# Kernel tuning notes

Hardware: AMD Instinct MI355X
Metric: run time of the kernel (lower is better)

The kernel has to match this reference:

```python
import jax, jax.numpy as jnp
import numpy as np

DIM = 768
HEADS = 12
HEAD_DIM = DIM // HEADS
SCALE = HEAD_DIM ** -0.5


def setup_inputs() -> dict:
    key = jax.random.key(0)
    ks = jax.random.split(key, 8)
    B, N, C = 8, 1024, DIM
    s = 0.02
    return {
        "x": jax.random.normal(ks[0], (B, N, C), jnp.float32),
        "y": jax.random.normal(ks[1], (B, N, C), jnp.float32),
        "x_qkv_w": jax.random.normal(ks[2], (3 * C, C), jnp.float32) * s,
        "y_qkv_w": jax.random.normal(ks[3], (3 * C, C), jnp.float32) * s,
        "x_proj_w": jax.random.normal(ks[4], (C, C), jnp.float32) * s,
        "x_proj_b": jnp.zeros((C,), jnp.float32),
        "y_proj_w": jax.random.normal(ks[5], (C, C), jnp.float32) * s,
        "y_proj_b": jnp.zeros((C,), jnp.float32),
    }


def _split_qkv(t, qkv_w):
    # t: [B,N,C] -> q,k,v each [B,H,N,D]
    B, N, C = t.shape
    qkv = t @ qkv_w.T                      # [B,N,3C]
    qkv = qkv.reshape(B, N, 3, HEADS, HEAD_DIM).transpose(2, 0, 3, 1, 4)
    return qkv[0], qkv[1], qkv[2]


def reference(x, y, x_qkv_w, y_qkv_w, x_proj_w, x_proj_b, y_proj_w, y_proj_b):
    B, N, C = x.shape
    x_q, x_k, x_v = _split_qkv(x, x_qkv_w)
    y_q, y_k, y_v = _split_qkv(y, y_qkv_w)

    # scores: [B,H,N,N]; dropout is identity (attn_drop=0)
    x_attn = jax.nn.softmax(jnp.einsum('bhnd,bhmd->bhnm', x_q * SCALE, x_k), axis=-1)
    y_attn = jax.nn.softmax(jnp.einsum('bhnd,bhmd->bhnm', y_q * SCALE, y_k), axis=-1)

    # swapped V aggregation: x-branch attends over y_v, y-branch over x_v
    x_out = jnp.einsum('bhnm,bhmd->bhnd', x_attn, y_v).transpose(0, 2, 1, 3).reshape(B, N, C)
    y_out = jnp.einsum('bhnm,bhmd->bhnd', y_attn, x_v).transpose(0, 2, 1, 3).reshape(B, N, C)

    x_out = x_out @ x_proj_w.T + x_proj_b
    y_out = y_out @ y_proj_w.T + y_proj_b
    return (x_out, y_out)
```

## Files before the change

### kernel.cpp

```cpp
#include <hip/hip_runtime.h>
#include <hip/hip_bf16.h>
#include <stdint.h>
#include <stddef.h>

typedef unsigned short u16;
typedef __attribute__((ext_vector_type(8))) short bf16x8;
typedef __attribute__((ext_vector_type(4))) short bf16x4;
typedef __attribute__((ext_vector_type(4))) float f32x4;
typedef __attribute__((ext_vector_type(4))) unsigned short u16x4;

#define MFMA_BF16 __builtin_amdgcn_mfma_f32_16x16x32_bf16

#if defined(__has_builtin)
#if __has_builtin(__builtin_amdgcn_mfma_f32_16x16x16bf16_1k)
#define MFMA16(a, b, c) __builtin_amdgcn_mfma_f32_16x16x16bf16_1k(a, b, c, 0, 0, 0)
#endif
#endif
#ifndef MFMA16
__device__ __forceinline__ f32x4 mfma16_asm(bf16x4 a, bf16x4 b, f32x4 c) {
  asm volatile("s_nop 1\n\tv_mfma_f32_16x16x16_bf16 %0, %1, %2, %0\n\ts_nop 7\n\ts_nop 7"
               : "+v"(c) : "v"(a), "v"(b));
  return c;
}
#define MFMA16(a, b, c) mfma16_asm(a, b, c)
#endif

#if defined(__has_builtin)
#if __has_builtin(__builtin_amdgcn_exp2f)
#define EXP2F(x) __builtin_amdgcn_exp2f(x)
#endif
#endif
#ifndef EXP2F
#define EXP2F(x) __expf((x) * 0.6931471805599453f)
#endif

#define BAR_FULL asm volatile("s_waitcnt vmcnt(0)\n\ts_barrier" ::: "memory")

#define QSCALE 0.18033688011112042f

__device__ __forceinline__ u16 f2b(float x) {
  uint32_t u = __builtin_bit_cast(uint32_t, x);
  return (u16)((u + 0x7fffu + ((u >> 16) & 1u)) >> 16);
}

__device__ __forceinline__ bf16x4 pack4(float a, float b, float c, float d) {
  union { __hip_bfloat162 h[2]; bf16x4 v; } u;
  u.h[0] = __float22bfloat162_rn(make_float2(a, b));
  u.h[1] = __float22bfloat162_rn(make_float2(c, d));
  return u.v;
}

__device__ __forceinline__ void async16(const void* g, void* l) {
  __builtin_amdgcn_global_load_lds((const __attribute__((address_space(1))) void*)g,
                                   (__attribute__((address_space(3))) void*)l, 16, 0, 0);
}

__global__ void cvt_all(const float* __restrict__ x, const float* __restrict__ y,
                        const float* __restrict__ xqw, const float* __restrict__ yqw,
                        const float* __restrict__ xpw, const float* __restrict__ ypw,
                        u16* __restrict__ dst) {
  long i = ((long)blockIdx.x * 256 + threadIdx.x) * 4;
  const float* src;
  long off;
  if (i < 6291456)       { src = x;   off = 0; }
  else if (i < 12582912) { src = y;   off = 6291456; }
  else if (i < 14352384) { src = xqw; off = 12582912; }
  else if (i < 16121856) { src = yqw; off = 14352384; }
  else if (i < 16711680) { src = xpw; off = 16121856; }
  else                   { src = ypw; off = 16711680; }
  float4 v = *(const float4*)(src + (i - off));
  u16x4 o = { f2b(v.x), f2b(v.y), f2b(v.z), f2b(v.w) };
  *(u16x4*)(dst + i) = o;
}

__global__ __launch_bounds__(256, 2)
void qkv_gemm(const u16* __restrict__ Xb, const u16* __restrict__ Yb,
              const u16* __restrict__ Wx, const u16* __restrict__ Wy,
              u16* __restrict__ Qx, u16* __restrict__ Kx, u16* __restrict__ Vtx,
              u16* __restrict__ Qy, u16* __restrict__ Ky, u16* __restrict__ Vty) {
  __shared__ alignas(16) char smem[65536];
  const int br = blockIdx.z;
  const u16* A = br ? Yb : Xb;
  const u16* W = br ? Wy : Wx;
  u16* Qd = br ? Qy : Qx;
  u16* Kd = br ? Ky : Kx;
  u16* Vd = br ? Vty : Vtx;
  const int m0 = blockIdx.x * 128;
  const int j0 = blockIdx.y * 128;
  const int tid = threadIdx.x;
  const int wave = tid >> 6, lane = tid & 63;
  const int quad = lane >> 4, l16 = lane & 15;
  const int wm = wave >> 1, wn = wave & 1;
  const int srow = wave * 32 + (lane >> 3);
  const int scol = (((lane & 7) ^ ((lane >> 3) & 7)) * 8);
  const int l7 = l16 & 7;

  auto stage = [&](int k0, int p) {
#pragma unroll
    for (int c = 0; c < 4; ++c) {
      async16(A + (size_t)(m0 + srow + c * 8) * 768 + k0 + scol,
              smem + p * 16384 + wave * 4096 + c * 1024);
      async16(W + (size_t)(j0 + srow + c * 8) * 768 + k0 + scol,
              smem + 32768 + p * 16384 + wave * 4096 + c * 1024);
    }
  };

  f32x4 acc[4][4] = {};
  stage(0, 0);

  for (int kt = 0; kt < 12; ++kt) {
    const int p = kt & 1;
    BAR_FULL;
    if (kt < 11) stage((kt + 1) * 64, p ^ 1);
    const u16* Ap = (const u16*)smem + p * 8192;
    const u16* Bp = (const u16*)smem + 16384 + p * 8192;
#pragma unroll
    for (int kc = 0; kc < 2; ++kc) {
      bf16x8 af[4], bfr[4];
#pragma unroll
      for (int t = 0; t < 4; ++t) {
        af[t]  = *(const bf16x8*)&Ap[(wm * 64 + t * 16 + l16) * 64 + (((kc * 4 + quad) ^ l7) * 8)];
        bfr[t] = *(const bf16x8*)&Bp[(wn * 64 + t * 16 + l16) * 64 + (((kc * 4 + quad) ^ l7) * 8)];
      }
#pragma unroll
      for (int mt = 0; mt < 4; ++mt)
#pragma unroll
        for (int nt = 0; nt < 4; ++nt)
          acc[mt][nt] = MFMA_BF16(af[mt], bfr[nt], acc[mt][nt], 0, 0, 0);
    }
  }

  __syncthreads();
  u16* Ts = (u16*)smem;
  const int s3 = j0 / 768;

  if (s3 == 2) {
#pragma unroll
    for (int mt = 0; mt < 4; ++mt)
#pragma unroll
      for (int nt = 0; nt < 4; ++nt) {
        const int j = wn * 64 + nt * 16 + l16;
        const int mb = wm * 64 + mt * 16 + quad * 4;
        u16x4 pk = { f2b(acc[mt][nt][0]), f2b(acc[mt][nt][1]),
                     f2b(acc[mt][nt][2]), f2b(acc[mt][nt][3]) };
        *(u16x4*)&Ts[j * 136 + mb] = pk;
      }
    __syncthreads();
#pragma unroll
    for (int rt = 0; rt < 8; ++rt) {
      const int j = wave * 32 + rt * 4 + (lane >> 4);
      const int mo = (lane & 15) * 8;
      bf16x8 v = *(const bf16x8*)&Ts[j * 136 + mo];
      const int jr = j0 + j - 1536;
      const int h = jr >> 6, d = jr & 63;
      const int gm = m0 + mo;
      const int b = gm >> 10, n = gm & 1023;
      *(bf16x8*)&Vd[((size_t)(b * 12 + h) * 64 + d) * 1024 + n] = v;
    }
  } else {
    const float qs = s3 ? 1.0f : QSCALE;
#pragma unroll
    for (int mt = 0; mt < 4; ++mt)
#pragma unroll
      for (int nt = 0; nt < 4; ++nt) {
        const int j = wn * 64 + nt * 16 + l16;
#pragma unroll
        for (int r = 0; r < 4; ++r) {
          const int m = wm * 64 + mt * 16 + quad * 4 + r;
          Ts[m * 136 + j] = f2b(acc[mt][nt][r] * qs);
        }
      }
    __syncthreads();
    u16* Dd = s3 ? Kd : Qd;
#pragma unroll
    for (int rt = 0; rt < 8; ++rt) {
      const int m = wave * 32 + rt * 4 + (lane >> 4);
      const int jh = (lane >> 3) & 1, jo = (lane & 7) * 8;
      bf16x8 v = *(const bf16x8*)&Ts[m * 136 + jh * 64 + jo];
      const int jr = j0 + jh * 64 + jo - s3 * 768;
      const int h = jr >> 6, d = jr & 63;
      const int gm = m0 + m;
      const int b = gm >> 10, n = gm & 1023;
      *(bf16x8*)&Dd[((size_t)(b * 12 + h) * 1024 + n) * 64 + d] = v;
    }
  }
}

__global__ __launch_bounds__(256, 2)
void attn_kernel(const u16* __restrict__ Qx, const u16* __restrict__ Kx, const u16* __restrict__ Vtx,
                 const u16* __restrict__ Qy, const u16* __restrict__ Ky, const u16* __restrict__ Vty,
                 u16* __restrict__ Ox, u16* __restrict__ Oy) {
  __shared__ alignas(16) u16 Ks[2][64 * 64];
  __shared__ alignas(16) u16 Vs[2][64 * 64];
  const int br = blockIdx.z;
  const u16* Q = br ? Qy : Qx;
  const u16* K = br ? Ky : Kx;
  const u16* V = br ? Vtx : Vty;
  u16* O = br ? Oy : Ox;
  const int bh = blockIdx.y;
  const int q0 = blockIdx.x * 256;
  const int tid = threadIdx.x;
  const int wave = tid >> 6, lane = tid & 63;
  const int quad = lane >> 4, l16 = lane & 15;
  const int l7 = l16 & 7;
  const int r8 = (lane >> 3) & 7;
  const int sw = ((lane & 7) ^ r8) * 8;

  const u16* Qb = Q + (size_t)bh * 65536;
  const u16* Kb = K + (size_t)bh * 65536;
  const u16* Vb = V + (size_t)bh * 65536;

  bf16x8 qf[4][2];
#pragma unroll
  for (int mt = 0; mt < 4; ++mt)
#pragma unroll
    for (int kc = 0; kc < 2; ++kc)
      qf[mt][kc] = *(const bf16x8*)(Qb + (size_t)(q0 + wave * 64 + mt * 16 + l16) * 64 + kc * 32 + quad * 8);

  f32x4 oacc[4][4] = {};
  f32x4 lsum[4] = {};
  bf16x4 ones4;
#pragma unroll
  for (int j = 0; j < 4; ++j) ones4[j] = (short)0x3f80;

  const int krow = wave * 16 + r8;

#pragma unroll
  for (int c = 0; c < 2; ++c) {
    async16(Kb + (size_t)(krow + c * 8) * 64 + sw, (char*)Ks[0] + wave * 2048 + c * 1024);
    async16(Vb + (size_t)(krow + c * 8) * 1024 + sw, (char*)Vs[0] + wave * 2048 + c * 1024);
  }

  for (int it = 0; it < 16; ++it) {
    const int p = it & 1;
    BAR_FULL;
    if (it < 15) {
      const int kv1 = (it + 1) * 64;
#pragma unroll
      for (int c = 0; c < 2; ++c) {
        async16(Kb + (size_t)(kv1 + krow + c * 8) * 64 + sw, (char*)Ks[p ^ 1] + wave * 2048 + c * 1024);
        async16(Vb + (size_t)(krow + c * 8) * 1024 + kv1 + sw, (char*)Vs[p ^ 1] + wave * 2048 + c * 1024);
      }
    }

    const u16* Kp = Ks[p];
    const u16* Vp = Vs[p];

#pragma unroll
    for (int kt = 0; kt < 4; ++kt) {
      f32x4 st[4] = {};
#pragma unroll
      for (int kc = 0; kc < 2; ++kc) {
        bf16x8 kf = *(const bf16x8*)&Kp[(kt * 16 + l16) * 64 + (((kc * 4 + quad) ^ l7) * 8)];
#pragma unroll
        for (int mt = 0; mt < 4; ++mt)
          st[mt] = MFMA_BF16(kf, qf[mt][kc], st[mt], 0, 0, 0);
      }
      bf16x4 pf[4];
#pragma unroll
      for (int mt = 0; mt < 4; ++mt)
        pf[mt] = pack4(EXP2F(st[mt][0]), EXP2F(st[mt][1]),
                       EXP2F(st[mt][2]), EXP2F(st[mt][3]));
      bf16x4 vf[4];
      const int c16 = kt * 2 + (quad >> 1);
      const int hh = (quad & 1) * 4;
#pragma unroll
      for (int dt = 0; dt < 4; ++dt)
        vf[dt] = *(const bf16x4*)&Vp[(dt * 16 + l16) * 64 + ((c16 ^ l7) * 8) + hh];
#pragma unroll
      for (int mt = 0; mt < 4; ++mt) {
#pragma unroll
        for (int dt = 0; dt < 4; ++dt)
          oacc[mt][dt] = MFMA16(pf[mt], vf[dt], oacc[mt][dt]);
        lsum[mt] = MFMA16(pf[mt], ones4, lsum[mt]);
      }
    }
  }

  const int b = bh / 12, h = bh % 12;
#pragma unroll
  for (int mt = 0; mt < 4; ++mt) {
#pragma unroll
    for (int r = 0; r < 4; ++r) {
      const float inv = 1.0f / lsum[mt][r];
      const int qrow = q0 + wave * 64 + mt * 16 + quad * 4 + r;
      const size_t ob = ((size_t)(b * 1024 + qrow)) * 768 + h * 64;
#pragma unroll
      for (int nt = 0; nt < 4; ++nt)
        O[ob + nt * 16 + l16] = f2b(oacc[mt][nt][r] * inv);
    }
  }
}

__global__ __launch_bounds__(256, 2)
void proj_gemm(const u16* __restrict__ Ox, const u16* __restrict__ Oy,
               const u16* __restrict__ Pxw, const u16* __restrict__ Pyw,
               const float* __restrict__ bx, const float* __restrict__ by,
               float* __restrict__ out) {
  __shared__ alignas(16) char smem[65536];
  const int br = blockIdx.z;
  const u16* A = br ? Oy : Ox;
  const u16* W = br ? Pyw : Pxw;
  const float* bias = br ? by : bx;
  float* op = out + (size_t)br * 6291456;
  const int m0 = blockIdx.x * 128;
  const int j0 = blockIdx.y * 128;
  const int tid = threadIdx.x;
  const int wave = tid >> 6, lane = tid & 63;
  const int quad = lane >> 4, l16 = lane & 15;
  const int wm = wave >> 1, wn = wave & 1;
  const int srow = wave * 32 + (lane >> 3);
  const int scol = (((lane & 7) ^ ((lane >> 3) & 7)) * 8);
  const int l7 = l16 & 7;

  auto stage = [&](int k0, int p) {
#pragma unroll
    for (int c = 0; c < 4; ++c) {
      async16(A + (size_t)(m0 + srow + c * 8) * 768 + k0 + scol,
              smem + p * 16384 + wave * 4096 + c * 1024);
      async16(W + (size_t)(j0 + srow + c * 8) * 768 + k0 + scol,
              smem + 32768 + p * 16384 + wave * 4096 + c * 1024);
    }
  };

  f32x4 acc[4][4] = {};
  stage(0, 0);

  for (int kt = 0; kt < 12; ++kt) {
    const int p = kt & 1;
    BAR_FULL;
    if (kt < 11) stage((kt + 1) * 64, p ^ 1);
    const u16* Ap = (const u16*)smem + p * 8192;
    const u16* Bp = (const u16*)smem + 16384 + p * 8192;
#pragma unroll
    for (int kc = 0; kc < 2; ++kc) {
      bf16x8 af[4], bfr[4];
#pragma unroll
      for (int t = 0; t < 4; ++t) {
        af[t]  = *(const bf16x8*)&Ap[(wm * 64 + t * 16 + l16) * 64 + (((kc * 4 + quad) ^ l7) * 8)];
        bfr[t] = *(const bf16x8*)&Bp[(wn * 64 + t * 16 + l16) * 64 + (((kc * 4 + quad) ^ l7) * 8)];
      }
#pragma unroll
      for (int mt = 0; mt < 4; ++mt)
#pragma unroll
        for (int nt = 0; nt < 4; ++nt)
          acc[mt][nt] = MFMA_BF16(af[mt], bfr[nt], acc[mt][nt], 0, 0, 0);
    }
  }

#pragma unroll
  for (int mt = 0; mt < 4; ++mt) {
#pragma unroll
    for (int nt = 0; nt < 4; ++nt) {
      const int j = j0 + wn * 64 + nt * 16 + l16;
      const float bj = bias[j];
#pragma unroll
      for (int r = 0; r < 4; ++r) {
        const int m = m0 + wm * 64 + mt * 16 + quad * 4 + r;
        op[(size_t)m * 768 + j] = acc[mt][nt][r] + bj;
      }
    }
  }
}

extern "C" void kernel_launch(void* const* d_in, const int* in_sizes, int n_in,
                              void* d_out, int out_size, void* d_ws, size_t ws_size,
                              hipStream_t stream) {
  (void)in_sizes; (void)n_in; (void)out_size; (void)ws_size;
  const float* x   = (const float*)d_in[0];
  const float* y   = (const float*)d_in[1];
  const float* xqw = (const float*)d_in[2];
  const float* yqw = (const float*)d_in[3];
  const float* xpw = (const float*)d_in[4];
  const float* xpb = (const float*)d_in[5];
  const float* ypw = (const float*)d_in[6];
  const float* ypb = (const float*)d_in[7];
  float* out = (float*)d_out;

  char* p = (char*)d_ws;
  u16* Xb  = (u16*)p; p += 12582912;
  u16* Yb  = (u16*)p; p += 12582912;
  u16* Wxb = (u16*)p; p += 3538944;
  u16* Wyb = (u16*)p; p += 3538944;
  u16* Pxb = (u16*)p; p += 1179648;
  u16* Pyb = (u16*)p; p += 1179648;
  u16* Qx  = (u16*)p; p += 12582912;
  u16* Kx  = (u16*)p; p += 12582912;
  u16* Vtx = (u16*)p; p += 12582912;
  u16* Qy  = (u16*)p; p += 12582912;
  u16* Ky  = (u16*)p; p += 12582912;
  u16* Vty = (u16*)p; p += 12582912;
  u16* Ox  = Xb;
  u16* Oy  = Yb;

  cvt_all<<<16896, 256, 0, stream>>>(x, y, xqw, yqw, xpw, ypw, Xb);

  qkv_gemm<<<dim3(64, 18, 2), 256, 0, stream>>>(Xb, Yb, Wxb, Wyb,
                                                Qx, Kx, Vtx, Qy, Ky, Vty);
  attn_kernel<<<dim3(4, 96, 2), 256, 0, stream>>>(Qx, Kx, Vtx, Qy, Ky, Vty, Ox, Oy);
  proj_gemm<<<dim3(64, 6, 2), 256, 0, stream>>>(Ox, Oy, Pxb, Pyb, xpb, ypb, out);
}
```

Baseline: 275.6 us.

## Switch attention kernel to 32x32x16 MFMA with permlane32 swap fragment reshuffle

Rewrites the attention inner loop to use 32x32x16 bf16 MFMA for both QK^T and PV instead of 16x16x32 plus 16x16x16. The exp'd scores are repacked into A-operand layout with v_permlane32_swap rather than being fed directly. The row sum is computed with VALU adds instead of an extra MFMA against a ones vector, then reduced across half-waves and shared through LDS. Launch bounds are raised to 3 blocks per CU to increase occupancy. The larger MFMA tiles are meant to cut instruction count and LDS fragment loads, at the cost of shuffle overhead and more register pressure under the tighter occupancy bound.

```diff
diff --git a/kernel.cpp b/kernel.cpp
--- a/kernel.cpp
+++ b/kernel.cpp
@@ -7,23 +7,11 @@
 typedef __attribute__((ext_vector_type(8))) short bf16x8;
 typedef __attribute__((ext_vector_type(4))) short bf16x4;
 typedef __attribute__((ext_vector_type(4))) float f32x4;
+typedef __attribute__((ext_vector_type(16))) float f32x16;
 typedef __attribute__((ext_vector_type(4))) unsigned short u16x4;
 
 #define MFMA_BF16 __builtin_amdgcn_mfma_f32_16x16x32_bf16
-
-#if defined(__has_builtin)
-#if __has_builtin(__builtin_amdgcn_mfma_f32_16x16x16bf16_1k)
-#define MFMA16(a, b, c) __builtin_amdgcn_mfma_f32_16x16x16bf16_1k(a, b, c, 0, 0, 0)
-#endif
-#endif
-#ifndef MFMA16
-__device__ __forceinline__ f32x4 mfma16_asm(bf16x4 a, bf16x4 b, f32x4 c) {
-  asm volatile("s_nop 1\n\tv_mfma_f32_16x16x16_bf16 %0, %1, %2, %0\n\ts_nop 7\n\ts_nop 7"
-               : "+v"(c) : "v"(a), "v"(b));
-  return c;
-}
-#define MFMA16(a, b, c) mfma16_asm(a, b, c)
-#endif
+#define MFMA32    __builtin_amdgcn_mfma_f32_32x32x16_bf16
 
 #if defined(__has_builtin)
 #if __has_builtin(__builtin_amdgcn_exp2f)
@@ -34,6 +22,17 @@
 #define EXP2F(x) __expf((x) * 0.6931471805599453f)
 #endif
 
+__device__ __forceinline__ void pl32swap(unsigned& a, unsigned& b) {
+#if defined(__has_builtin) && __has_builtin(__builtin_amdgcn_permlane32_swap)
+  typedef int v2i __attribute__((ext_vector_type(2)));
+  v2i r = __builtin_amdgcn_permlane32_swap((int)a, (int)b, false, false);
+  a = (unsigned)r.x;
+  b = (unsigned)r.y;
+#else
+  asm volatile("v_permlane32_swap_b32 %0, %1" : "+v"(a), "+v"(b));
+#endif
+}
+
 #define BAR_FULL asm volatile("s_waitcnt vmcnt(0)\n\ts_barrier" ::: "memory")
 
 #define QSCALE 0.18033688011112042f
@@ -43,11 +42,10 @@
   return (u16)((u + 0x7fffu + ((u >> 16) & 1u)) >> 16);
 }
 
-__device__ __forceinline__ bf16x4 pack4(float a, float b, float c, float d) {
-  union { __hip_bfloat162 h[2]; bf16x4 v; } u;
-  u.h[0] = __float22bfloat162_rn(make_float2(a, b));
-  u.h[1] = __float22bfloat162_rn(make_float2(c, d));
-  return u.v;
+__device__ __forceinline__ unsigned pk2(float a, float b) {
+  union { __hip_bfloat162 h; unsigned u; } c;
+  c.h = __float22bfloat162_rn(make_float2(a, b));
+  return c.u;
 }
 
 __device__ __forceinline__ void async16(const void* g, void* l) {
@@ -186,7 +184,7 @@
   }
 }
 
-__global__ __launch_bounds__(256, 2)
+__global__ __launch_bounds__(256, 3)
 void attn_kernel(const u16* __restrict__ Qx, const u16* __restrict__ Kx, const u16* __restrict__ Vtx,
                  const u16* __restrict__ Qy, const u16* __restrict__ Ky, const u16* __restrict__ Vty,
                  u16* __restrict__ Ox, u16* __restrict__ Oy) {
@@ -201,8 +199,8 @@
   const int q0 = blockIdx.x * 256;
   const int tid = threadIdx.x;
   const int wave = tid >> 6, lane = tid & 63;
-  const int quad = lane >> 4, l16 = lane & 15;
-  const int l7 = l16 & 7;
+  const int l = lane & 31, hi = lane >> 5;
+  const int l7 = lane & 7;
   const int r8 = (lane >> 3) & 7;
   const int sw = ((lane & 7) ^ r8) * 8;
 
@@ -210,19 +208,6 @@
   const u16* Kb = K + (size_t)bh * 65536;
   const u16* Vb = V + (size_t)bh * 65536;
 
-  bf16x8 qf[4][2];
-#pragma unroll
-  for (int mt = 0; mt < 4; ++mt)
-#pragma unroll
-    for (int kc = 0; kc < 2; ++kc)
-      qf[mt][kc] = *(const bf16x8*)(Qb + (size_t)(q0 + wave * 64 + mt * 16 + l16) * 64 + kc * 32 + quad * 8);
-
-  f32x4 oacc[4][4] = {};
-  f32x4 lsum[4] = {};
-  bf16x4 ones4;
-#pragma unroll
-  for (int j = 0; j < 4; ++j) ones4[j] = (short)0x3f80;
-
   const int krow = wave * 16 + r8;
 
 #pragma unroll
@@ -230,6 +215,18 @@
     async16(Kb + (size_t)(krow + c * 8) * 64 + sw, (char*)Ks[0] + wave * 2048 + c * 1024);
     async16(Vb + (size_t)(krow + c * 8) * 1024 + sw, (char*)Vs[0] + wave * 2048 + c * 1024);
   }
+
+  bf16x8 qf[2][4];
+#pragma unroll
+  for (int qh = 0; qh < 2; ++qh)
+#pragma unroll
+    for (int dc = 0; dc < 4; ++dc)
+      qf[qh][dc] = *(const bf16x8*)(Qb + (size_t)(q0 + wave * 64 + qh * 32 + l) * 64 + dc * 16 + hi * 8);
+
+  f32x16 oacc[2][2] = {};
+  float lsum[2] = {0.f, 0.f};
+
+  union FrU { unsigned u[4]; bf16x8 v; };
 
   for (int it = 0; it < 16; ++it) {
     const int p = it & 1;
@@ -247,49 +244,72 @@
     const u16* Vp = Vs[p];
 
 #pragma unroll
-    for (int kt = 0; kt < 4; ++kt) {
-      f32x4 st[4] = {};
-#pragma unroll
-      for (int kc = 0; kc < 2; ++kc) {
-        bf16x8 kf = *(const bf16x8*)&Kp[(kt * 16 + l16) * 64 + (((kc * 4 + quad) ^ l7) * 8)];
-#pragma unroll
-        for (int mt = 0; mt < 4; ++mt)
-          st[mt] = MFMA_BF16(kf, qf[mt][kc], st[mt], 0, 0, 0);
-      }
-      bf16x4 pf[4];
-#pragma unroll
-      for (int mt = 0; mt < 4; ++mt)
-        pf[mt] = pack4(EXP2F(st[mt][0]), EXP2F(st[mt][1]),
-                       EXP2F(st[mt][2]), EXP2F(st[mt][3]));
-      bf16x4 vf[4];
-      const int c16 = kt * 2 + (quad >> 1);
-      const int hh = (quad & 1) * 4;
-#pragma unroll
-      for (int dt = 0; dt < 4; ++dt)
-        vf[dt] = *(const bf16x4*)&Vp[(dt * 16 + l16) * 64 + ((c16 ^ l7) * 8) + hh];
-#pragma unroll
-      for (int mt = 0; mt < 4; ++mt) {
-#pragma unroll
-        for (int dt = 0; dt < 4; ++dt)
-          oacc[mt][dt] = MFMA16(pf[mt], vf[dt], oacc[mt][dt]);
-        lsum[mt] = MFMA16(pf[mt], ones4, lsum[mt]);
-      }
-    }
-  }
+    for (int s = 0; s < 2; ++s) {
+      bf16x8 kf[4];
+#pragma unroll
+      for (int dc = 0; dc < 4; ++dc)
+        kf[dc] = *(const bf16x8*)&Kp[(s * 32 + l) * 64 + (((dc * 2 + hi) ^ l7) * 8)];
+
+      FrU fragA[2][2];
+#pragma unroll
+      for (int qh = 0; qh < 2; ++qh) {
+        f32x16 st = {};
+#pragma unroll
+        for (int dc = 0; dc < 4; ++dc)
+          st = MFMA32(kf[dc], qf[qh][dc], st, 0, 0, 0);
+        float pv[16];
+#pragma unroll
+        for (int r = 0; r < 16; ++r) pv[r] = EXP2F(st[r]);
+        lsum[qh] += (((pv[0] + pv[1]) + (pv[2] + pv[3])) + ((pv[4] + pv[5]) + (pv[6] + pv[7])))
+                  + (((pv[8] + pv[9]) + (pv[10] + pv[11])) + ((pv[12] + pv[13]) + (pv[14] + pv[15])));
+        unsigned P[8];
+#pragma unroll
+        for (int i = 0; i < 8; ++i) P[i] = pk2(pv[2 * i], pv[2 * i + 1]);
+#pragma unroll
+        for (int f = 0; f < 2; ++f) {
+          unsigned a0 = P[f * 4 + 0], b0 = P[f * 4 + 2];
+          unsigned a1 = P[f * 4 + 1], b1 = P[f * 4 + 3];
+          pl32swap(a0, b0);
+          pl32swap(a1, b1);
+          fragA[qh][f].u[0] = a0;
+          fragA[qh][f].u[1] = a1;
+          fragA[qh][f].u[2] = b0;
+          fragA[qh][f].u[3] = b1;
+        }
+      }
+#pragma unroll
+      for (int f = 0; f < 2; ++f)
+#pragma unroll
+        for (int dt = 0; dt < 2; ++dt) {
+          bf16x8 vf = *(const bf16x8*)&Vp[(dt * 32 + l) * 64 + (((s * 4 + f * 2 + hi) ^ l7) * 8)];
+          oacc[0][dt] = MFMA32(fragA[0][f].v, vf, oacc[0][dt], 0, 0, 0);
+          oacc[1][dt] = MFMA32(fragA[1][f].v, vf, oacc[1][dt], 0, 0, 0);
+        }
+    }
+  }
+
+  float* LS = (float*)Ks[0] + wave * 64;
+  {
+    float t0 = lsum[0] + __shfl_xor(lsum[0], 32, 64);
+    float t1 = lsum[1] + __shfl_xor(lsum[1], 32, 64);
+    LS[l] = 1.0f / t0;
+    LS[32 + l] = 1.0f / t1;
+  }
+  __syncthreads();
 
   const int b = bh / 12, h = bh % 12;
 #pragma unroll
-  for (int mt = 0; mt < 4; ++mt) {
-#pragma unroll
-    for (int r = 0; r < 4; ++r) {
-      const float inv = 1.0f / lsum[mt][r];
-      const int qrow = q0 + wave * 64 + mt * 16 + quad * 4 + r;
+  for (int qh = 0; qh < 2; ++qh)
+#pragma unroll
+    for (int r = 0; r < 16; ++r) {
+      const int cr = (r & 3) + 8 * (r >> 2) + 4 * hi;
+      const float iv = LS[qh * 32 + cr];
+      const int qrow = q0 + wave * 64 + qh * 32 + cr;
       const size_t ob = ((size_t)(b * 1024 + qrow)) * 768 + h * 64;
 #pragma unroll
-      for (int nt = 0; nt < 4; ++nt)
-        O[ob + nt * 16 + l16] = f2b(oacc[mt][nt][r] * inv);
-    }
-  }
+      for (int dt = 0; dt < 2; ++dt)
+        O[ob + dt * 32 + l] = f2b(oacc[qh][dt][r] * iv);
+    }
 }
 
 __global__ __launch_bounds__(256, 2)
```

Result: slower. 320.9 us (+16.4%).
